# Kernel optimization log

Measured on AMD Instinct MI355X. Metric: run time of the kernel, lower is better.

Reference implementation:

```python
import jax, jax.numpy as jnp
import numpy as np

N_PTS = 131072
IN_CH = 63
IN_CH_VIEWS = 27
WIDTH = 256
NUM_HEADS = 4
SCALE = 0.05


def setup_inputs() -> dict:
    key = jax.random.key(0)
    ks = jax.random.split(key, 12)
    H, W = NUM_HEADS, WIDTH
    inp = {
        'x': jax.random.normal(ks[0], (N_PTS, IN_CH + IN_CH_VIEWS), jnp.float32),
        'head_idx': jax.random.randint(ks[1], (N_PTS,), 0, NUM_HEADS),
        # shared trunk: layer0 63->256, layers1..3 256->256 (no skip before split_at=4)
        'W0': jax.random.normal(ks[2], (IN_CH, W), jnp.float32) * SCALE,
        'b0': jnp.zeros((W,), jnp.float32),
        'Ws': jax.random.normal(ks[3], (3, W, W), jnp.float32) * SCALE,
        'bs': jnp.zeros((3, W), jnp.float32),
        # per-head tails: g=4 in skips -> (W+63)->W, then g=5..7 W->W
        'tW0': jax.random.normal(ks[4], (H, W + IN_CH, W), jnp.float32) * SCALE,
        'tb0': jnp.zeros((H, W), jnp.float32),
        'tWs': jax.random.normal(ks[5], (H, 3, W, W), jnp.float32) * SCALE,
        'tbs': jnp.zeros((H, 3, W), jnp.float32),
        # per-head viewdirs output heads
        'featW': jax.random.normal(ks[6], (H, W, W), jnp.float32) * SCALE,
        'featb': jnp.zeros((H, W), jnp.float32),
        'alphaW': jax.random.normal(ks[7], (H, W, 1), jnp.float32) * SCALE,
        'alphab': jnp.zeros((H, 1), jnp.float32),
        'viewsW': jax.random.normal(ks[8], (H, IN_CH_VIEWS + W, W // 2), jnp.float32) * SCALE,
        'viewsb': jnp.zeros((H, W // 2), jnp.float32),
        'rgbW': jax.random.normal(ks[9], (H, W // 2, 3), jnp.float32) * SCALE,
        'rgbb': jnp.zeros((H, 3), jnp.float32),
    }
    return inp


def reference(x, head_idx, W0, b0, Ws, bs, tW0, tb0, tWs, tbs,
              featW, featb, alphaW, alphab, viewsW, viewsb, rgbW, rgbb):
    input_pts = x[:, :IN_CH]          # [N, 63]
    input_views = x[:, IN_CH:]        # [N, 27]

    # shared trunk (layers 0..3, no skip hits in this range)
    h = jax.nn.relu(input_pts @ W0 + b0)
    for i in range(Ws.shape[0]):
        h = jax.nn.relu(h @ Ws[i] + bs[i])

    # per-head tails, computed densely for ALL heads (as in the original)
    # first tail layer g=4 is a skip layer: concat input_pts
    ht = jnp.concatenate([input_pts, h], axis=-1)          # [N, 319]
    ha = jax.nn.relu(jnp.einsum('nf,hfo->nho', ht, tW0) + tb0[None])  # [N, H, 256]
    for j in range(tWs.shape[1]):
        ha = jax.nn.relu(jnp.einsum('nho,hop->nhp', ha, tWs[:, j]) + tbs[None, :, j])

    # per-head viewdir output heads
    alpha = jnp.einsum('nho,hop->nhp', ha, alphaW) + alphab[None]     # [N, H, 1]
    feat = jnp.einsum('nho,hop->nhp', ha, featW) + featb[None]        # [N, H, 256]
    views_b = jnp.broadcast_to(input_views[:, None, :], (x.shape[0], feat.shape[1], IN_CH_VIEWS))
    hv = jnp.concatenate([feat, views_b], axis=-1)                    # [N, H, 283]
    hv = jax.nn.relu(jnp.einsum('nho,hop->nhp', hv, viewsW) + viewsb[None])
    rgb = jnp.einsum('nho,hop->nhp', hv, rgbW) + rgbb[None]           # [N, H, 3]

    outs = jnp.concatenate([rgb, alpha], axis=-1)                     # [N, H, 4]
    sel = jnp.take_along_axis(outs, head_idx[:, None, None], axis=1)[:, 0]  # [N, 4]
    return sel
```

## Files before the change

kernel.cpp:

```cpp
#include <hip/hip_runtime.h>

#define N_PTS 131072
#define TILE 64
#define THREADS 512
#define REGION 40960

typedef __bf16 bf16;
typedef __bf16 bf16x8 __attribute__((ext_vector_type(8)));
typedef float f32x4 __attribute__((ext_vector_type(4)));

#define WS_PERM_OFF   256
#define WS_WPACK_OFF  (256 + 4 * REGION * 4)
#define OFF_W0     0
#define OFF_WS     16384
#define OFF_TW0    212992
#define OFF_TWS    540672
#define OFF_FEATW  1327104
#define OFF_VIEWSW 1589248
#define TOTAL_PACK 1736704

#define H_BASE 0
#define B_BASE 32768
#define LDS_BYTES 81920

__device__ __forceinline__ unsigned swz(unsigned base, unsigned row, unsigned rowstride,
                                        unsigned kbyte) {
  return (base + row * rowstride + kbyte) ^ ((row & 7u) << 4);
}

__device__ __forceinline__ void gload_lds16(const bf16* g, char* l) {
  __builtin_amdgcn_global_load_lds(
      (const __attribute__((address_space(1))) void*)g,
      (__attribute__((address_space(3))) void*)l, 16, 0, 0);
}

template <int N>
__device__ __forceinline__ void wait_stage() {
  if constexpr (N == 0)      asm volatile("s_waitcnt vmcnt(0)" ::: "memory");
  else if constexpr (N == 1) asm volatile("s_waitcnt vmcnt(1)" ::: "memory");
  else                       asm volatile("s_waitcnt vmcnt(2)" ::: "memory");
}

__global__ void k_pack(const float* __restrict__ W0, const float* __restrict__ Ws,
                       const float* __restrict__ tW0, const float* __restrict__ tWs,
                       const float* __restrict__ featW, const float* __restrict__ viewsW,
                       bf16* __restrict__ out, const int* __restrict__ head,
                       int* __restrict__ ctrl, int* __restrict__ perm) {
  int gid = blockIdx.x * blockDim.x + threadIdx.x;
  if (gid < N_PTS) {
    int h = head[gid];
    int lane = threadIdx.x & 63;
    #pragma unroll
    for (int hh = 0; hh < 4; ++hh) {
      unsigned long long m = __ballot(h == hh);
      if (m == 0ull) continue;
      int leader = __builtin_ctzll(m);
      int base = 0;
      if (lane == leader) base = atomicAdd(&ctrl[16 + hh], __popcll(m));
      base = __shfl(base, leader);
      if (h == hh) {
        int rank = __popcll(m & ((1ull << lane) - 1ull));
        perm[hh * REGION + base + rank] = gid;
      }
    }
  }

  for (int idx = gid; idx < TOTAL_PACK; idx += gridDim.x * blockDim.x) {
    float v; int dst;
    if (idx < 16384) {
      int k = idx >> 8, o = idx & 255;
      v = (k < 63) ? W0[k * 256 + o] : 0.f;
      dst = OFF_W0 + o * 64 + k;
    } else if (idx < 212992) {
      int i = idx - 16384; int l = i >> 16, r = i & 65535, k = r >> 8, o = r & 255;
      v = Ws[i];
      dst = OFF_WS + l * 65536 + o * 256 + k;
    } else if (idx < 540672) {
      int i = idx - 212992; int h = i / 81920, r = i % 81920, k = r >> 8, o = r & 255;
      v = (k < 63) ? tW0[(h * 319 + k) * 256 + o]
                   : (k == 63 ? 0.f : tW0[(h * 319 + k - 1) * 256 + o]);
      dst = OFF_TW0 + h * 81920 + o * 320 + k;
    } else if (idx < 1327104) {
      int i = idx - 540672; int hj = i >> 16, r = i & 65535, k = r >> 8, o = r & 255;
      v = tWs[i];
      dst = OFF_TWS + hj * 65536 + o * 256 + k;
    } else if (idx < 1589248) {
      int i = idx - 1327104; int h = i >> 16, r = i & 65535, k = r >> 8, o = r & 255;
      v = featW[i];
      dst = OFF_FEATW + h * 65536 + o * 256 + k;
    } else {
      int i = idx - 1589248; int h = i / 36864, r = i % 36864, k = r >> 7, o = r & 127;
      v = (k < 283) ? viewsW[(h * 283 + k) * 128 + o] : 0.f;
      dst = OFF_VIEWSW + h * 36864 + o * 288 + k;
    }
    out[dst] = (bf16)v;
  }
}

#define PIPE_STEP(WAITN, DO_STAGE, LOAD_A)                                     \
  do {                                                                         \
    wait_stage<WAITN>();                                                       \
    __builtin_amdgcn_s_barrier();                                              \
    if (DO_STAGE) {                                                            \
      _Pragma("unroll")                                                        \
      for (int s = 0; s < ISSUES; ++s) {                                       \
        gload_lds16(gsrc[s], sbase + sd + s * 1024);                           \
        gsrc[s] += 32;                                                         \
      }                                                                        \
      sd = (sd == 32768) ? 0 : sd + 16384;                                     \
    }                                                                          \
    bf16x8 a[MR];                                                              \
    LOAD_A;                                                                    \
    bf16x8 b[NF];                                                              \
    {                                                                          \
      const char* bp = lds + breg + sr;                                        \
      _Pragma("unroll")                                                        \
      for (int n = 0; n < NF; ++n) b[n] = *(const bf16x8*)(bp + n * 1024);     \
    }                                                                          \
    sr = (sr == 32768) ? 0 : sr + 16384;                                       \
    __builtin_amdgcn_s_setprio(1);                                             \
    _Pragma("unroll")                                                          \
    for (int n = 0; n < NF; ++n)                                               \
      _Pragma("unroll")                                                        \
      for (int m = 0; m < MR; ++m)                                             \
        acc[m][n] =                                                            \
            __builtin_amdgcn_mfma_f32_16x16x32_bf16(a[m], b[n], acc[m][n],     \
                                                    0, 0, 0);                  \
    __builtin_amdgcn_s_setprio(0);                                             \
  } while (0)

#define LOADA_REG(K)                                                           \
  { _Pragma("unroll") for (int m = 0; m < MR; ++m) a[m] = aregs[(K) * MR + m]; }

#define LOADA_LDS                                                              \
  {                                                                            \
    unsigned va = acur ^ axor;                                                 \
    _Pragma("unroll")                                                          \
    for (int m = 0; m < MR; ++m) a[m] = *(const bf16x8*)(lds + va + m * 8192); \
    acur += 64;                                                                \
  }

template <int MR, int NF, bool RELU, int RKC, int LKC, bool REG_FIRST, int OUTS>
__device__ __forceinline__ void mfma_layer(char* lds, const bf16* __restrict__ Wt,
                                           int wK, const float* __restrict__ bias,
                                           const bf16x8* aregs,
                                           int lane, int wave) {
  const int l15 = lane & 15, l4 = lane >> 4;
  const int wr = wave >> 2, wc = wave & 3;
  constexpr int KC = RKC + LKC;
  constexpr int ISSUES = OUTS / 128;
  f32x4 acc[MR][NF];
  #pragma unroll
  for (int m = 0; m < MR; ++m)
    #pragma unroll
    for (int n = 0; n < NF; ++n) acc[m][n] = (f32x4){0.f, 0.f, 0.f, 0.f};

  const int r0 = wr * (MR * 16);
  const int c0 = wc * (NF * 16);

  const int breg = B_BASE + (c0 + l15) * 64 + ((l4 ^ ((l15 >> 1) & 3)) << 4);

  unsigned acur = (unsigned)((r0 + l15) * 512 + l4 * 16);
  const unsigned axor = (l15 & 7u) << 4;

  const bf16* gsrc[ISSUES];
  #pragma unroll
  for (int s = 0; s < ISSUES; ++s) {
    int reg = wave * ISSUES + s;
    int o = reg * 16 + (lane >> 2);
    int j = lane & 3;
    gsrc[s] = Wt + o * wK + ((j ^ ((o >> 1) & 3)) << 3);
  }
  char* sbase = lds + B_BASE + (wave * ISSUES) * 1024;

  #pragma unroll
  for (int s = 0; s < ISSUES; ++s) { gload_lds16(gsrc[s], sbase + s * 1024); gsrc[s] += 32; }
  #pragma unroll
  for (int s = 0; s < ISSUES; ++s) { gload_lds16(gsrc[s], sbase + 16384 + s * 1024); gsrc[s] += 32; }

  int sr = 0;
  int sd = 32768;

  if constexpr (REG_FIRST && RKC >= 1) {
    if constexpr (KC == 1) PIPE_STEP(0, false, LOADA_REG(0));
    else                   PIPE_STEP(ISSUES, (2 < KC), LOADA_REG(0));
  }
  if constexpr (REG_FIRST && RKC >= 2) {
    if constexpr (KC == 2) PIPE_STEP(0, false, LOADA_REG(1));
    else                   PIPE_STEP(ISSUES, (3 < KC), LOADA_REG(1));
  }

  if constexpr (LKC > 0) {
    constexpr int kc0 = REG_FIRST ? RKC : 0;
    constexpr bool last_in_lds = (REG_FIRST || RKC == 0);
    constexpr int kcend = REG_FIRST ? KC : LKC;
    constexpr int loop_end = kcend - (last_in_lds ? 1 : 0);
    #pragma unroll 1
    for (int kc = kc0; kc < loop_end; ++kc) {
      PIPE_STEP(ISSUES, (kc + 2 < KC), LOADA_LDS);
    }
    if constexpr (last_in_lds) PIPE_STEP(0, false, LOADA_LDS);
  }

  if constexpr (!REG_FIRST && RKC >= 1) {
    PIPE_STEP(0, false, LOADA_REG(0));
  }

  __builtin_amdgcn_s_barrier();

  #pragma unroll
  for (int n = 0; n < NF; ++n) {
    int col = c0 + n * 16 + l15;
    float bv = bias[col];
    #pragma unroll
    for (int m = 0; m < MR; ++m) {
      #pragma unroll
      for (int j = 0; j < 4; ++j) {
        float v = acc[m][n][j] + bv;
        if (RELU) v = fmaxf(v, 0.f);
        int row = r0 + m * 16 + l4 * 4 + j;
        *(bf16*)(lds + swz(H_BASE, row, 512, col * 2)) = (bf16)v;
      }
    }
  }
  __syncthreads();
}

__global__ __launch_bounds__(THREADS, 4) void k_main(
    const float* __restrict__ x, const int* __restrict__ ctrl, const int* __restrict__ perm,
    const bf16* __restrict__ wpack,
    const float* __restrict__ b0, const float* __restrict__ bs,
    const float* __restrict__ tb0p, const float* __restrict__ tbsp,
    const float* __restrict__ featb, const float* __restrict__ alphaW,
    const float* __restrict__ alphab, const float* __restrict__ viewsb,
    const float* __restrict__ rgbW, const float* __restrict__ rgbb,
    float* __restrict__ outp) {
  __shared__ __attribute__((aligned(16))) char lds[LDS_BYTES];

  const int tid = threadIdx.x;
  const int lane = tid & 63, wave = tid >> 6;
  const int l15 = lane & 15, l4 = lane >> 4;

  const int hh = blockIdx.x / (REGION / TILE);
  const int start = (blockIdx.x % (REGION / TILE)) * TILE;
  const int cnt = ctrl[16 + hh];
  if (start >= cnt) return;
  const int nv = min(TILE, cnt - start);
  const int permbase = hh * REGION + start;

  bf16x8 ptsreg[4];
  bf16x8 viewsreg[2];
  {
    const int wr = wave >> 2;
    #pragma unroll
    for (int m = 0; m < 2; ++m) {
      int row = wr * 32 + m * 16 + l15;
      bool valid = (start + row) < cnt;
      int p = valid ? perm[permbase + row] : 0;
      const float* xr = x + p * 90;
      #pragma unroll
      for (int rkc = 0; rkc < 2; ++rkc) {
        int k0 = rkc * 32 + l4 * 8;
        bf16x8 f;
        #pragma unroll
        for (int j = 0; j < 8; ++j) {
          int k = k0 + j;
          f[j] = (bf16)((valid && k < 63) ? xr[k] : 0.f);
        }
        ptsreg[rkc * 2 + m] = f;
      }
      {
        int k0 = l4 * 8;
        bf16x8 f;
        #pragma unroll
        for (int j = 0; j < 8; ++j) {
          int k = k0 + j;
          f[j] = (bf16)((valid && k < 27) ? xr[63 + k] : 0.f);
        }
        viewsreg[m] = f;
      }
    }
  }

  const bf16* W0p    = wpack + OFF_W0;
  const bf16* Wsp    = wpack + OFF_WS;
  const bf16* tW0p   = wpack + OFF_TW0 + hh * 81920;
  const bf16* tWsp   = wpack + OFF_TWS + hh * 3 * 65536;
  const bf16* featWp = wpack + OFF_FEATW + hh * 65536;
  const bf16* viewsWp= wpack + OFF_VIEWSW + hh * 36864;

  mfma_layer<2, 4, true, 2, 0, true,  256>(lds, W0p, 64, b0, ptsreg, lane, wave);
  mfma_layer<2, 4, true, 0, 8, false, 256>(lds, Wsp,          256, bs,       nullptr, lane, wave);
  mfma_layer<2, 4, true, 0, 8, false, 256>(lds, Wsp + 65536,  256, bs + 256, nullptr, lane, wave);
  mfma_layer<2, 4, true, 0, 8, false, 256>(lds, Wsp + 131072, 256, bs + 512, nullptr, lane, wave);
  mfma_layer<2, 4, true, 2, 8, true,  256>(lds, tW0p, 320, tb0p + hh * 256, ptsreg, lane, wave);

  mfma_layer<2, 4, true, 0, 8, false, 256>(lds, tWsp,          256, tbsp + hh * 768,       nullptr, lane, wave);
  mfma_layer<2, 4, true, 0, 8, false, 256>(lds, tWsp + 65536,  256, tbsp + hh * 768 + 256, nullptr, lane, wave);
  mfma_layer<2, 4, true, 0, 8, false, 256>(lds, tWsp + 131072, 256, tbsp + hh * 768 + 512, nullptr, lane, wave);

  float my_alpha = 0.f;
  if (wave < 4) {
    int p = wave * 16 + l15;
    int kq = l4 >> 1;
    const float* aW = alphaW + hh * 256;
    float s = 0.f;
    int kqq = lane >> 4;
    for (int i = 0; i < 4; ++i) {
      int k = kqq * 64 + i * 16;
      bf16x8 h0 = *(const bf16x8*)(lds + swz(H_BASE, p, 512, k * 2));
      bf16x8 h1 = *(const bf16x8*)(lds + swz(H_BASE, p, 512, (k + 8) * 2));
      #pragma unroll
      for (int j = 0; j < 8; ++j) s += (float)h0[j] * aW[k + j];
      #pragma unroll
      for (int j = 0; j < 8; ++j) s += (float)h1[j] * aW[k + 8 + j];
    }
    s += __shfl_xor(s, 16);
    s += __shfl_xor(s, 32);
    my_alpha = s + alphab[hh];
    (void)kq;
  }

  mfma_layer<2, 4, false, 0, 8, false, 256>(lds, featWp, 256, featb + hh * 256, nullptr, lane, wave);
  mfma_layer<2, 2, true, 1, 8, false, 128>(lds, viewsWp, 288, viewsb + hh * 128, viewsreg, lane, wave);

  if (wave < 4) {
    int p = wave * 16 + l15;
    int kq = lane >> 4;
    const float* rW = rgbW + hh * 128 * 3;
    float r0 = 0.f, r1 = 0.f, r2 = 0.f;
    for (int i = 0; i < 4; ++i) {
      int k = kq * 32 + i * 8;
      bf16x8 hv8 = *(const bf16x8*)(lds + swz(H_BASE, p, 512, k * 2));
      #pragma unroll
      for (int j = 0; j < 8; ++j) {
        float hvf = (float)hv8[j];
        r0 += hvf * rW[(k + j) * 3 + 0];
        r1 += hvf * rW[(k + j) * 3 + 1];
        r2 += hvf * rW[(k + j) * 3 + 2];
      }
    }
    r0 += __shfl_xor(r0, 16); r0 += __shfl_xor(r0, 32);
    r1 += __shfl_xor(r1, 16); r1 += __shfl_xor(r1, 32);
    r2 += __shfl_xor(r2, 16); r2 += __shfl_xor(r2, 32);
    if (kq == 0 && p < nv) {
      int pt = perm[permbase + p];
      float4 o = make_float4(r0 + rgbb[hh * 3 + 0], r1 + rgbb[hh * 3 + 1],
                             r2 + rgbb[hh * 3 + 2], my_alpha);
      *(float4*)(outp + pt * 4) = o;
    }
  }
}

extern "C" void kernel_launch(void* const* d_in, const int* in_sizes, int n_in,
                              void* d_out, int out_size, void* d_ws, size_t ws_size,
                              hipStream_t stream) {
  const float* x      = (const float*)d_in[0];
  const int*   head   = (const int*)d_in[1];
  const float* W0     = (const float*)d_in[2];
  const float* b0     = (const float*)d_in[3];
  const float* Ws     = (const float*)d_in[4];
  const float* bs     = (const float*)d_in[5];
  const float* tW0    = (const float*)d_in[6];
  const float* tb0    = (const float*)d_in[7];
  const float* tWs    = (const float*)d_in[8];
  const float* tbs    = (const float*)d_in[9];
  const float* featW  = (const float*)d_in[10];
  const float* featb  = (const float*)d_in[11];
  const float* alphaW = (const float*)d_in[12];
  const float* alphab = (const float*)d_in[13];
  const float* viewsW = (const float*)d_in[14];
  const float* viewsb = (const float*)d_in[15];
  const float* rgbW   = (const float*)d_in[16];
  const float* rgbb   = (const float*)d_in[17];

  int*  ctrl  = (int*)d_ws;
  int*  perm  = (int*)((char*)d_ws + WS_PERM_OFF);
  bf16* wpack = (bf16*)((char*)d_ws + WS_WPACK_OFF);

  hipMemsetAsync(ctrl, 0, 256, stream);
  k_pack<<<2048, 256, 0, stream>>>(W0, Ws, tW0, tWs, featW, viewsW, wpack, head, ctrl, perm);
  k_main<<<4 * (REGION / TILE), THREADS, 0, stream>>>(x, ctrl, perm, wpack,
                                                      b0, bs, tb0, tbs, featb, alphaW, alphab,
                                                      viewsb, rgbW, rgbb, (float*)d_out);
}
```

Measured before the change: 392.8 us.

## Use 4-wave blocks with per-wave private weight staging, removing per-step barriers

```diff
diff --git a/kernel.cpp b/kernel.cpp
--- a/kernel.cpp
+++ b/kernel.cpp
@@ -2,7 +2,7 @@
 
 #define N_PTS 131072
 #define TILE 64
-#define THREADS 512
+#define THREADS 256
 #define REGION 40960
 
 typedef __bf16 bf16;
@@ -35,10 +35,8 @@
 }
 
 template <int N>
-__device__ __forceinline__ void wait_stage() {
-  if constexpr (N == 0)      asm volatile("s_waitcnt vmcnt(0)" ::: "memory");
-  else if constexpr (N == 1) asm volatile("s_waitcnt vmcnt(1)" ::: "memory");
-  else                       asm volatile("s_waitcnt vmcnt(2)" ::: "memory");
+__device__ __forceinline__ void wait_vm() {
+  asm volatile("s_waitcnt vmcnt(%0)" ::"n"(N) : "memory");
 }
 
 __global__ void k_pack(const float* __restrict__ W0, const float* __restrict__ Ws,
@@ -97,128 +95,100 @@
   }
 }
 
-#define PIPE_STEP(WAITN, DO_STAGE, LOAD_A)                                     \
-  do {                                                                         \
-    wait_stage<WAITN>();                                                       \
-    __builtin_amdgcn_s_barrier();                                              \
-    if (DO_STAGE) {                                                            \
-      _Pragma("unroll")                                                        \
-      for (int s = 0; s < ISSUES; ++s) {                                       \
-        gload_lds16(gsrc[s], sbase + sd + s * 1024);                           \
-        gsrc[s] += 32;                                                         \
-      }                                                                        \
-      sd = (sd == 32768) ? 0 : sd + 16384;                                     \
-    }                                                                          \
-    bf16x8 a[MR];                                                              \
-    LOAD_A;                                                                    \
-    bf16x8 b[NF];                                                              \
-    {                                                                          \
-      const char* bp = lds + breg + sr;                                        \
-      _Pragma("unroll")                                                        \
-      for (int n = 0; n < NF; ++n) b[n] = *(const bf16x8*)(bp + n * 1024);     \
-    }                                                                          \
-    sr = (sr == 32768) ? 0 : sr + 16384;                                       \
-    __builtin_amdgcn_s_setprio(1);                                             \
-    _Pragma("unroll")                                                          \
-    for (int n = 0; n < NF; ++n)                                               \
-      _Pragma("unroll")                                                        \
-      for (int m = 0; m < MR; ++m)                                             \
-        acc[m][n] =                                                            \
-            __builtin_amdgcn_mfma_f32_16x16x32_bf16(a[m], b[n], acc[m][n],     \
-                                                    0, 0, 0);                  \
-    __builtin_amdgcn_s_setprio(0);                                             \
-  } while (0)
-
-#define LOADA_REG(K)                                                           \
-  { _Pragma("unroll") for (int m = 0; m < MR; ++m) a[m] = aregs[(K) * MR + m]; }
-
-#define LOADA_LDS                                                              \
-  {                                                                            \
-    unsigned va = acur ^ axor;                                                 \
-    _Pragma("unroll")                                                          \
-    for (int m = 0; m < MR; ++m) a[m] = *(const bf16x8*)(lds + va + m * 8192); \
-    acur += 64;                                                                \
-  }
-
-template <int MR, int NF, bool RELU, int RKC, int LKC, bool REG_FIRST, int OUTS>
+template <int NF, bool RELU, int RKC, int LKC, bool REG_FIRST, int OUTS>
 __device__ __forceinline__ void mfma_layer(char* lds, const bf16* __restrict__ Wt,
                                            int wK, const float* __restrict__ bias,
-                                           const bf16x8* aregs,
-                                           int lane, int wave) {
+                                           const bf16x8* aregs, int lane, int wave) {
   const int l15 = lane & 15, l4 = lane >> 4;
-  const int wr = wave >> 2, wc = wave & 3;
   constexpr int KC = RKC + LKC;
-  constexpr int ISSUES = OUTS / 128;
-  f32x4 acc[MR][NF];
-  #pragma unroll
-  for (int m = 0; m < MR; ++m)
+  f32x4 acc[4][NF];
+  #pragma unroll
+  for (int m = 0; m < 4; ++m)
     #pragma unroll
     for (int n = 0; n < NF; ++n) acc[m][n] = (f32x4){0.f, 0.f, 0.f, 0.f};
 
-  const int r0 = wr * (MR * 16);
-  const int c0 = wc * (NF * 16);
-
-  const int breg = B_BASE + (c0 + l15) * 64 + ((l4 ^ ((l15 >> 1) & 3)) << 4);
-
-  unsigned acur = (unsigned)((r0 + l15) * 512 + l4 * 16);
+  const int c0 = wave * (NF * 16);
+  const int wbase = B_BASE + wave * 12288;
+
+  float bv[NF];
+  #pragma unroll
+  for (int n = 0; n < NF; ++n) bv[n] = bias[c0 + n * 16 + l15];
+
+  const int breg = wbase + l15 * 64 + ((l4 ^ ((l15 >> 1) & 3)) << 4);
+
+  unsigned acur = (unsigned)(l15 * 512 + l4 * 16);
   const unsigned axor = (l15 & 7u) << 4;
 
-  const bf16* gsrc[ISSUES];
-  #pragma unroll
-  for (int s = 0; s < ISSUES; ++s) {
-    int reg = wave * ISSUES + s;
-    int o = reg * 16 + (lane >> 2);
+  const bf16* gsrc[NF];
+  #pragma unroll
+  for (int s = 0; s < NF; ++s) {
+    int op = s * 16 + (lane >> 2);
     int j = lane & 3;
-    gsrc[s] = Wt + o * wK + ((j ^ ((o >> 1) & 3)) << 3);
-  }
-  char* sbase = lds + B_BASE + (wave * ISSUES) * 1024;
-
-  #pragma unroll
-  for (int s = 0; s < ISSUES; ++s) { gload_lds16(gsrc[s], sbase + s * 1024); gsrc[s] += 32; }
-  #pragma unroll
-  for (int s = 0; s < ISSUES; ++s) { gload_lds16(gsrc[s], sbase + 16384 + s * 1024); gsrc[s] += 32; }
-
-  int sr = 0;
-  int sd = 32768;
-
-  if constexpr (REG_FIRST && RKC >= 1) {
-    if constexpr (KC == 1) PIPE_STEP(0, false, LOADA_REG(0));
-    else                   PIPE_STEP(ISSUES, (2 < KC), LOADA_REG(0));
-  }
-  if constexpr (REG_FIRST && RKC >= 2) {
-    if constexpr (KC == 2) PIPE_STEP(0, false, LOADA_REG(1));
-    else                   PIPE_STEP(ISSUES, (3 < KC), LOADA_REG(1));
-  }
-
-  if constexpr (LKC > 0) {
-    constexpr int kc0 = REG_FIRST ? RKC : 0;
-    constexpr bool last_in_lds = (REG_FIRST || RKC == 0);
-    constexpr int kcend = REG_FIRST ? KC : LKC;
-    constexpr int loop_end = kcend - (last_in_lds ? 1 : 0);
-    #pragma unroll 1
-    for (int kc = kc0; kc < loop_end; ++kc) {
-      PIPE_STEP(ISSUES, (kc + 2 < KC), LOADA_LDS);
-    }
-    if constexpr (last_in_lds) PIPE_STEP(0, false, LOADA_LDS);
-  }
-
-  if constexpr (!REG_FIRST && RKC >= 1) {
-    PIPE_STEP(0, false, LOADA_REG(0));
-  }
+    gsrc[s] = Wt + (c0 + op) * wK + ((j ^ ((op >> 1) & 3)) << 3);
+  }
+
+  #pragma unroll
+  for (int s = 0; s < NF; ++s) { gload_lds16(gsrc[s], lds + wbase + s * 1024); gsrc[s] += 32; }
+  #pragma unroll
+  for (int s = 0; s < NF; ++s) { gload_lds16(gsrc[s], lds + wbase + 4096 + s * 1024); gsrc[s] += 32; }
+
+  int rd = 0, st = 8192;
+
+  auto dostep = [&](int kc, const bf16x8* ar) {
+    if (kc + 2 < KC) {
+      #pragma unroll
+      for (int s = 0; s < NF; ++s) { gload_lds16(gsrc[s], lds + wbase + st + s * 1024); gsrc[s] += 32; }
+      st = (st == 8192) ? 0 : st + 4096;
+      wait_vm<2 * NF>();
+    } else if (kc + 1 < KC) {
+      wait_vm<NF>();
+    } else {
+      wait_vm<0>();
+    }
+
+    bf16x8 a[4];
+    if (ar) {
+      #pragma unroll
+      for (int m = 0; m < 4; ++m) a[m] = ar[m];
+    } else {
+      unsigned va = acur ^ axor;
+      #pragma unroll
+      for (int m = 0; m < 4; ++m) a[m] = *(const bf16x8*)(lds + va + m * 8192);
+      acur += 64;
+    }
+    bf16x8 b[NF];
+    #pragma unroll
+    for (int n = 0; n < NF; ++n) b[n] = *(const bf16x8*)(lds + breg + rd + n * 1024);
+    rd = (rd == 8192) ? 0 : rd + 4096;
+
+    __builtin_amdgcn_s_setprio(1);
+    #pragma unroll
+    for (int n = 0; n < NF; ++n)
+      #pragma unroll
+      for (int m = 0; m < 4; ++m)
+        acc[m][n] = __builtin_amdgcn_mfma_f32_16x16x32_bf16(a[m], b[n], acc[m][n], 0, 0, 0);
+    __builtin_amdgcn_s_setprio(0);
+  };
+
+  if constexpr (REG_FIRST && RKC >= 1) dostep(0, aregs);
+  if constexpr (REG_FIRST && RKC >= 2) dostep(1, aregs + 4);
+  #pragma unroll 1
+  for (int kc = (REG_FIRST ? RKC : 0); kc < (REG_FIRST ? KC : LKC); ++kc)
+    dostep(kc, nullptr);
+  if constexpr (!REG_FIRST && RKC >= 1) dostep(KC - 1, aregs);
 
   __builtin_amdgcn_s_barrier();
 
   #pragma unroll
   for (int n = 0; n < NF; ++n) {
     int col = c0 + n * 16 + l15;
-    float bv = bias[col];
-    #pragma unroll
-    for (int m = 0; m < MR; ++m) {
+    #pragma unroll
+    for (int m = 0; m < 4; ++m) {
       #pragma unroll
       for (int j = 0; j < 4; ++j) {
-        float v = acc[m][n][j] + bv;
+        float v = acc[m][n][j] + bv[n];
         if (RELU) v = fmaxf(v, 0.f);
-        int row = r0 + m * 16 + l4 * 4 + j;
+        int row = m * 16 + l4 * 4 + j;
         *(bf16*)(lds + swz(H_BASE, row, 512, col * 2)) = (bf16)v;
       }
     }
@@ -226,7 +196,7 @@
   __syncthreads();
 }
 
-__global__ __launch_bounds__(THREADS, 4) void k_main(
+__global__ __launch_bounds__(THREADS, 2) void k_main(
     const float* __restrict__ x, const int* __restrict__ ctrl, const int* __restrict__ perm,
     const bf16* __restrict__ wpack,
     const float* __restrict__ b0, const float* __restrict__ bs,
@@ -248,37 +218,34 @@
   const int nv = min(TILE, cnt - start);
   const int permbase = hh * REGION + start;
 
-  bf16x8 ptsreg[4];
-  bf16x8 viewsreg[2];
-  {
-    const int wr = wave >> 2;
-    #pragma unroll
-    for (int m = 0; m < 2; ++m) {
-      int row = wr * 32 + m * 16 + l15;
-      bool valid = (start + row) < cnt;
-      int p = valid ? perm[permbase + row] : 0;
-      const float* xr = x + p * 90;
-      #pragma unroll
-      for (int rkc = 0; rkc < 2; ++rkc) {
-        int k0 = rkc * 32 + l4 * 8;
-        bf16x8 f;
-        #pragma unroll
-        for (int j = 0; j < 8; ++j) {
-          int k = k0 + j;
-          f[j] = (bf16)((valid && k < 63) ? xr[k] : 0.f);
-        }
-        ptsreg[rkc * 2 + m] = f;
-      }
-      {
-        int k0 = l4 * 8;
-        bf16x8 f;
-        #pragma unroll
-        for (int j = 0; j < 8; ++j) {
-          int k = k0 + j;
-          f[j] = (bf16)((valid && k < 27) ? xr[63 + k] : 0.f);
-        }
-        viewsreg[m] = f;
-      }
+  bf16x8 ptsreg[8];
+  bf16x8 viewsreg[4];
+  #pragma unroll
+  for (int m = 0; m < 4; ++m) {
+    int row = m * 16 + l15;
+    bool valid = (start + row) < cnt;
+    int p = valid ? perm[permbase + row] : 0;
+    const float* xr = x + p * 90;
+    #pragma unroll
+    for (int rkc = 0; rkc < 2; ++rkc) {
+      int k0 = rkc * 32 + l4 * 8;
+      bf16x8 f;
+      #pragma unroll
+      for (int j = 0; j < 8; ++j) {
+        int k = k0 + j;
+        f[j] = (bf16)((valid && k < 63) ? xr[k] : 0.f);
+      }
+      ptsreg[rkc * 4 + m] = f;
+    }
+    {
+      int k0 = l4 * 8;
+      bf16x8 f;
+      #pragma unroll
+      for (int j = 0; j < 8; ++j) {
+        int k = k0 + j;
+        f[j] = (bf16)((valid && k < 27) ? xr[63 + k] : 0.f);
+      }
+      viewsreg[m] = f;
     }
   }
 
@@ -289,42 +256,37 @@
   const bf16* featWp = wpack + OFF_FEATW + hh * 65536;
   const bf16* viewsWp= wpack + OFF_VIEWSW + hh * 36864;
 
-  mfma_layer<2, 4, true, 2, 0, true,  256>(lds, W0p, 64, b0, ptsreg, lane, wave);
-  mfma_layer<2, 4, true, 0, 8, false, 256>(lds, Wsp,          256, bs,       nullptr, lane, wave);
-  mfma_layer<2, 4, true, 0, 8, false, 256>(lds, Wsp + 65536,  256, bs + 256, nullptr, lane, wave);
-  mfma_layer<2, 4, true, 0, 8, false, 256>(lds, Wsp + 131072, 256, bs + 512, nullptr, lane, wave);
-  mfma_layer<2, 4, true, 2, 8, true,  256>(lds, tW0p, 320, tb0p + hh * 256, ptsreg, lane, wave);
-
-  mfma_layer<2, 4, true, 0, 8, false, 256>(lds, tWsp,          256, tbsp + hh * 768,       nullptr, lane, wave);
-  mfma_layer<2, 4, true, 0, 8, false, 256>(lds, tWsp + 65536,  256, tbsp + hh * 768 + 256, nullptr, lane, wave);
-  mfma_layer<2, 4, true, 0, 8, false, 256>(lds, tWsp + 131072, 256, tbsp + hh * 768 + 512, nullptr, lane, wave);
-
-  float my_alpha = 0.f;
-  if (wave < 4) {
+  mfma_layer<4, true, 2, 0, true,  256>(lds, W0p, 64, b0, ptsreg, lane, wave);
+  mfma_layer<4, true, 0, 8, false, 256>(lds, Wsp,          256, bs,       nullptr, lane, wave);
+  mfma_layer<4, true, 0, 8, false, 256>(lds, Wsp + 65536,  256, bs + 256, nullptr, lane, wave);
+  mfma_layer<4, true, 0, 8, false, 256>(lds, Wsp + 131072, 256, bs + 512, nullptr, lane, wave);
+  mfma_layer<4, true, 2, 8, true,  256>(lds, tW0p, 320, tb0p + hh * 256, ptsreg, lane, wave);
+
+  mfma_layer<4, true, 0, 8, false, 256>(lds, tWsp,          256, tbsp + hh * 768,       nullptr, lane, wave);
+  mfma_layer<4, true, 0, 8, false, 256>(lds, tWsp + 65536,  256, tbsp + hh * 768 + 256, nullptr, lane, wave);
+  mfma_layer<4, true, 0, 8, false, 256>(lds, tWsp + 131072, 256, tbsp + hh * 768 + 512, nullptr, lane, wave);
+
+  float my_alpha;
+  {
     int p = wave * 16 + l15;
-    int kq = l4 >> 1;
+    int kq = lane >> 4;
     const float* aW = alphaW + hh * 256;
     float s = 0.f;
-    int kqq = lane >> 4;
-    for (int i = 0; i < 4; ++i) {
-      int k = kqq * 64 + i * 16;
-      bf16x8 h0 = *(const bf16x8*)(lds + swz(H_BASE, p, 512, k * 2));
-      bf16x8 h1 = *(const bf16x8*)(lds + swz(H_BASE, p, 512, (k + 8) * 2));
-      #pragma unroll
-      for (int j = 0; j < 8; ++j) s += (float)h0[j] * aW[k + j];
-      #pragma unroll
-      for (int j = 0; j < 8; ++j) s += (float)h1[j] * aW[k + 8 + j];
+    for (int i = 0; i < 8; ++i) {
+      int k = kq * 64 + i * 8;
+      bf16x8 hv8 = *(const bf16x8*)(lds + swz(H_BASE, p, 512, k * 2));
+      #pragma unroll
+      for (int j = 0; j < 8; ++j) s += (float)hv8[j] * aW[k + j];
     }
     s += __shfl_xor(s, 16);
     s += __shfl_xor(s, 32);
     my_alpha = s + alphab[hh];
-    (void)kq;
-  }
-
-  mfma_layer<2, 4, false, 0, 8, false, 256>(lds, featWp, 256, featb + hh * 256, nullptr, lane, wave);
-  mfma_layer<2, 2, true, 1, 8, false, 128>(lds, viewsWp, 288, viewsb + hh * 128, viewsreg, lane, wave);
-
-  if (wave < 4) {
+  }
+
+  mfma_layer<4, false, 0, 8, false, 256>(lds, featWp, 256, featb + hh * 256, nullptr, lane, wave);
+  mfma_layer<2, true, 1, 8, false, 128>(lds, viewsWp, 288, viewsb + hh * 128, viewsreg, lane, wave);
+
+  {
     int p = wave * 16 + l15;
     int kq = lane >> 4;
     const float* rW = rgbW + hh * 128 * 3;
```

Measured after the change: 422.1 us. 1.07x slower.
